# Optimization experiments

Hardware: AMD Instinct MI355X
Metric: run time of the kernel (lower is better)

## Reference

```python
import jax, jax.numpy as jnp
import numpy as np

N_NODES = 50000
N_EDGES = 800000
D_NODE = 128
D_EDGE = 16
HID = 128
BN_EPS = 1e-5


def gcn_conv(h, src, dst, W, b):
    # PyG GCNConv: h' = D^-1/2 (A + I) D^-1/2 (h W) + b, deg includes self-loop
    h = h @ W
    deg = jax.ops.segment_sum(jnp.ones((src.shape[0],), h.dtype), dst,
                              num_segments=N_NODES) + 1.0
    dinv = deg ** -0.5
    norm = dinv[src] * dinv[dst]                      # [E]
    agg = jax.ops.segment_sum(h[src] * norm[:, None], dst,
                              num_segments=N_NODES)   # scatter to dst
    agg = agg + h * (dinv * dinv)[:, None]            # self-loop term
    return agg + b


def setup_inputs() -> dict:
    key = jax.random.key(0)
    ks = jax.random.split(key, 12)
    s = lambda fan_in: 1.0 / np.sqrt(fan_in)
    return {
        "x": jax.random.normal(ks[0], (N_NODES, D_NODE), jnp.float32),
        "edge_index": jax.random.randint(ks[1], (2, N_EDGES), 0, N_NODES, jnp.int32),
        "edge_attr": jax.random.normal(ks[2], (N_EDGES, D_EDGE), jnp.float32),
        "W1": jax.random.normal(ks[3], (D_NODE, HID), jnp.float32) * s(D_NODE),
        "b1": jnp.zeros((HID,), jnp.float32),
        "gamma": jnp.ones((HID,), jnp.float32),
        "beta": jnp.zeros((HID,), jnp.float32),
        "W2": jax.random.normal(ks[4], (HID, HID), jnp.float32) * s(HID),
        "b2": jnp.zeros((HID,), jnp.float32),
        "Wm1": jax.random.normal(ks[5], (2 * HID + D_EDGE, HID), jnp.float32) * s(2 * HID + D_EDGE),
        "bm1": jnp.zeros((HID,), jnp.float32),
        "Wm2": jax.random.normal(ks[6], (HID, 1), jnp.float32) * s(HID),
        "bm2": jnp.zeros((1,), jnp.float32),
    }


def reference(x, edge_index, edge_attr, W1, b1, gamma, beta, W2, b2, Wm1, bm1, Wm2, bm2):
    src, dst = edge_index[0], edge_index[1]
    z = gcn_conv(x, src, dst, W1, b1)
    # BatchNorm1d over nodes (training-mode batch stats, biased var)
    mean = jnp.mean(z, axis=0)
    var = jnp.mean(jnp.square(z - mean), axis=0)
    z = (z - mean) * jax.lax.rsqrt(var + BN_EPS) * gamma + beta
    z = jax.nn.relu(z)
    z = gcn_conv(z, src, dst, W2, b2)
    # edge head: gather endpoints, concat with edge_attr, 2-layer MLP (dropout = eval identity)
    edge_input = jnp.concatenate([z[src], z[dst], edge_attr], axis=1)  # [E, 2H+De]
    h = jax.nn.relu(edge_input @ Wm1 + bm1)
    return (h @ Wm2 + bm2).squeeze(-1)  # [E]
```

## Files before the change

kernel.cpp:

```cpp
#include <hip/hip_runtime.h>
#include <hip/hip_bf16.h>

#define NN 50000
#define NE 800000
#define H 128
#define DE 16
#define BN_EPS 1e-5f
#define NBKT 196
#define NBLK 256
#define EPB 3125
#define EHB 1563

typedef float v2f __attribute__((ext_vector_type(2)));
typedef float v4f __attribute__((ext_vector_type(4)));
typedef short bfrag __attribute__((ext_vector_type(8)));

__device__ __forceinline__ unsigned int packbf2(float a, float b) {
    __hip_bfloat162 h = __float22bfloat162_rn(make_float2(a, b));
    return *(unsigned int*)&h;
}
__device__ __forceinline__ v2f unpackbf2(unsigned int u) {
    v2f r;
    r.x = __uint_as_float(u << 16);
    r.y = __uint_as_float(u & 0xffff0000u);
    return r;
}
__device__ __forceinline__ bfrag cvt8(float4 a0, float4 a1) {
    union { uint4 u; bfrag f; } x;
    x.u.x = packbf2(a0.x, a0.y);
    x.u.y = packbf2(a0.z, a0.w);
    x.u.z = packbf2(a1.x, a1.y);
    x.u.w = packbf2(a1.z, a1.w);
    return x.f;
}
__device__ __forceinline__ bfrag cvt8v(v4f a0, v4f a1) {
    union { uint4 u; bfrag f; } x;
    x.u.x = packbf2(a0.x, a0.y);
    x.u.y = packbf2(a0.z, a0.w);
    x.u.z = packbf2(a1.x, a1.y);
    x.u.w = packbf2(a1.z, a1.w);
    return x.f;
}
#define COMP(u4, j) ((j) == 0 ? (u4).x : (j) == 1 ? (u4).y : (j) == 2 ? (u4).z : (u4).w)

__device__ __forceinline__ float dpp_rowred16(float s) {
    s += __int_as_float(__builtin_amdgcn_update_dpp(0, __float_as_int(s), 0x121, 0xf, 0xf, false));
    s += __int_as_float(__builtin_amdgcn_update_dpp(0, __float_as_int(s), 0x122, 0xf, 0xf, false));
    s += __int_as_float(__builtin_amdgcn_update_dpp(0, __float_as_int(s), 0x124, 0xf, 0xf, false));
    s += __int_as_float(__builtin_amdgcn_update_dpp(0, __float_as_int(s), 0x128, 0xf, 0xf, false));
    return s;
}

__global__ __launch_bounds__(256) void phaseA_k(const int* __restrict__ dst,
                                                int* __restrict__ bhist,
                                                const float* __restrict__ W1,
                                                const float* __restrict__ W2,
                                                const float* __restrict__ Ws,
                                                const float* __restrict__ Wd,
                                                const float* __restrict__ We,
                                                short* __restrict__ d1, short* __restrict__ d2,
                                                short* __restrict__ ds_, short* __restrict__ dd,
                                                unsigned int* __restrict__ WePk) {
    int b = blockIdx.x;
    if (b < NBLK) {
        __shared__ int lh[256];
        lh[threadIdx.x] = 0;
        __syncthreads();
        int base = b * EPB;
        for (int e = threadIdx.x; e < EPB; e += 256)
            atomicAdd(&lh[dst[base + e] >> 8], 1);
        __syncthreads();
        if (threadIdx.x < NBKT)
            bhist[threadIdx.x * NBLK + b] = lh[threadIdx.x];
        return;
    }
    b -= NBLK;
    if (b < 256) {
        int mat = b >> 6;
        const float* s = mat == 0 ? W1 : mat == 1 ? W2 : mat == 2 ? Ws : Wd;
        short* d = mat == 0 ? d1 : mat == 1 ? d2 : mat == 2 ? ds_ : dd;
        int idx = (b & 63) * 256 + threadIdx.x;
        int n = idx & 127, k = idx >> 7;
        float v = s[k * 128 + n];
        d[n * 128 + k] = (short)(packbf2(v, v) & 0xffff);
    } else {
        int idx = (b - 256) * 256 + threadIdx.x;
        int c = idx >> 8;
        int lane = (idx >> 2) & 63;
        int j2 = (idx & 3) * 2;
        int q = lane >> 4, i = lane & 15;
        int k0 = q * 8 + j2, k1 = k0 + 1;
        int feat = i * 8 + c;
        float v0 = (k0 < 16) ? We[k0 * 128 + feat] : 0.f;
        float v1 = (k1 < 16) ? We[k1 * 128 + feat] : 0.f;
        WePk[idx] = packbf2(v0, v1);
    }
}

__global__ void phaseB_k(int* __restrict__ bhist, int* __restrict__ bucketBase,
                         int* __restrict__ bucketTot) {
    __shared__ int sh[256];
    int t = threadIdx.x;
    int tot = 0;
    if (t < NBKT)
        for (int blk = 0; blk < NBLK; blk++) tot += bhist[t * NBLK + blk];
    sh[t] = tot;
    __syncthreads();
    for (int off = 1; off < 256; off <<= 1) {
        int v = (t >= off) ? sh[t - off] : 0;
        __syncthreads();
        sh[t] += v;
        __syncthreads();
    }
    if (t < NBKT) {
        int base = sh[t] - tot;
        bucketBase[t] = base;
        bucketTot[t] = tot;
        int run = base;
        for (int blk = 0; blk < NBLK; blk++) {
            int h = bhist[t * NBLK + blk];
            bhist[t * NBLK + blk] = run;
            run += h;
        }
    }
}

__global__ __launch_bounds__(512) void phaseC_k(const int* __restrict__ src,
                                                const int* __restrict__ dst,
                                                const int* __restrict__ bhist,
                                                unsigned int* __restrict__ tmp) {
    __shared__ int lcur[256];
    int b = blockIdx.x;
    if (threadIdx.x < NBKT)
        lcur[threadIdx.x] = bhist[threadIdx.x * NBLK + b];
    __syncthreads();
    int base = b * EPB;
    for (int e = threadIdx.x; e < EPB; e += 512) {
        int d = dst[base + e];
        int s = src[base + e];
        int pos = atomicAdd(&lcur[d >> 8], 1);
        tmp[pos] = (unsigned int)s | ((unsigned int)(d & 255) << 16);
    }
}

__global__ __launch_bounds__(512) void fillb_k(const int* __restrict__ bucketBase,
                                               const int* __restrict__ bucketTot,
                                               const unsigned int* __restrict__ tmp,
                                               int* __restrict__ counts,
                                               int* __restrict__ offsets,
                                               float* __restrict__ dinv,
                                               int* __restrict__ srcs) {
    __shared__ int hist[256], off[256];
    int t = threadIdx.x;
    int b = blockIdx.x;
    if (t < 256) hist[t] = 0;
    __syncthreads();
    int base = bucketBase[b];
    int tot = bucketTot[b];
    const unsigned int* tp = tmp + base;
    for (int idx = t; idx < tot; idx += 512)
        atomicAdd(&hist[tp[idx] >> 16], 1);
    __syncthreads();
    int h = 0;
    if (t < 256) { h = hist[t]; off[t] = h; }
    __syncthreads();
    for (int o = 1; o < 256; o <<= 1) {
        int v = (t < 256 && t >= o) ? off[t - o] : 0;
        __syncthreads();
        if (t < 256) off[t] += v;
        __syncthreads();
    }
    if (t < 256) {
        int excl = off[t] - h;
        int node = b * 256 + t;
        if (node < NN) {
            counts[node] = h;
            offsets[node] = base + excl;
            dinv[node] = rsqrtf((float)h + 1.0f);
        }
        hist[t] = excl;
    }
    __syncthreads();
    for (int idx = t; idx < tot; idx += 512) {
        unsigned int u = tp[idx];
        int pos = atomicAdd(&hist[u >> 16], 1);
        srcs[base + pos] = (int)(u & 0xffffu);
    }
}

__global__ __launch_bounds__(256) void gemm1_k(const float* __restrict__ A,
                                               const short* __restrict__ Bt,
                                               unsigned int* __restrict__ Cb,
                                               const float* __restrict__ rowScale) {
    int lane = threadIdx.x & 63;
    int w = threadIdx.x >> 6;
    int i = lane & 15;
    int q = lane >> 4;
    int r0 = blockIdx.x * 64 + w * 16;
    int arow = min(r0 + i, NN - 1);
    const float* Arow = A + (size_t)arow * 128;

    v4f acc[8];
#pragma unroll
    for (int c = 0; c < 8; c++) acc[c] = (v4f)0.f;

#pragma unroll
    for (int kc = 0; kc < 128; kc += 32) {
        int kb = kc + q * 8;
        float4 a0 = *(const float4*)&Arow[kb];
        float4 a1 = *(const float4*)&Arow[kb + 4];
        bfrag af = cvt8(a0, a1);
#pragma unroll
        for (int c = 0; c < 8; c++) {
            bfrag bf = *(const bfrag*)&Bt[(size_t)(c * 16 + i) * 128 + kb];
            acc[c] = __builtin_amdgcn_mfma_f32_16x16x32_bf16(af, bf, acc[c], 0, 0, 0);
        }
    }

    int orow0 = r0 + q * 4;
    v4f ds = *(const v4f*)&rowScale[min(orow0, NN - 4)];
#pragma unroll
    for (int c = 0; c < 8; c++) {
        int col = c * 16 + i;
#pragma unroll
        for (int r = 0; r < 4; r++) {
            float v = acc[c][r] * ds[r];
            float vp = __shfl_xor(v, 1, 64);
            if (!(i & 1) && orow0 + r < NN)
                Cb[(size_t)(orow0 + r) * 64 + (col >> 1)] = packbf2(v, vp);
        }
    }
}

__global__ __launch_bounds__(256) void gemm_bn_k(const unsigned int* __restrict__ Ab,
                                                 const short* __restrict__ Bt,
                                                 unsigned int* __restrict__ Cb,
                                                 const float* __restrict__ rowScale,
                                                 const float* __restrict__ sums,
                                                 const float* __restrict__ sumsq,
                                                 const float* __restrict__ gamma,
                                                 const float* __restrict__ beta) {
    __shared__ __align__(16) float tAs[128], tCs[128];
    if (threadIdx.x < 128) {
        int f = threadIdx.x;
        float mean = sums[f] * (1.0f / NN);
        float var = sumsq[f] * (1.0f / NN) - mean * mean;
        float a = gamma[f] * rsqrtf(var + BN_EPS);
        tAs[f] = a;
        tCs[f] = beta[f] - mean * a;
    }
    __syncthreads();

    int lane = threadIdx.x & 63;
    int w = threadIdx.x >> 6;
    int i = lane & 15;
    int q = lane >> 4;
    int r0 = blockIdx.x * 64 + w * 16;
    int arow = min(r0 + i, NN - 1);

    v4f acc[8];
#pragma unroll
    for (int c = 0; c < 8; c++) acc[c] = (v4f)0.f;

#pragma unroll
    for (int kc = 0; kc < 128; kc += 32) {
        int kb = kc + q * 8;
        uint4 u = *(const uint4*)&Ab[(size_t)arow * 64 + (kb >> 1)];
        v2f z0 = unpackbf2(u.x), z1 = unpackbf2(u.y);
        v2f z2 = unpackbf2(u.z), z3 = unpackbf2(u.w);
        v2f t0 = *(const v2f*)&tAs[kb],     c0 = *(const v2f*)&tCs[kb];
        v2f t1 = *(const v2f*)&tAs[kb + 2], c1 = *(const v2f*)&tCs[kb + 2];
        v2f t2 = *(const v2f*)&tAs[kb + 4], c2 = *(const v2f*)&tCs[kb + 4];
        v2f t3 = *(const v2f*)&tAs[kb + 6], c3 = *(const v2f*)&tCs[kb + 6];
        z0 = z0 * t0 + c0; z1 = z1 * t1 + c1;
        z2 = z2 * t2 + c2; z3 = z3 * t3 + c3;
        union { uint4 u; bfrag f; } x;
        x.u.x = packbf2(fmaxf(z0.x, 0.f), fmaxf(z0.y, 0.f));
        x.u.y = packbf2(fmaxf(z1.x, 0.f), fmaxf(z1.y, 0.f));
        x.u.z = packbf2(fmaxf(z2.x, 0.f), fmaxf(z2.y, 0.f));
        x.u.w = packbf2(fmaxf(z3.x, 0.f), fmaxf(z3.y, 0.f));
        bfrag af = x.f;
#pragma unroll
        for (int c = 0; c < 8; c++) {
            bfrag bf = *(const bfrag*)&Bt[(size_t)(c * 16 + i) * 128 + kb];
            acc[c] = __builtin_amdgcn_mfma_f32_16x16x32_bf16(af, bf, acc[c], 0, 0, 0);
        }
    }

    int orow0 = r0 + q * 4;
    v4f ds = *(const v4f*)&rowScale[min(orow0, NN - 4)];
#pragma unroll
    for (int c = 0; c < 8; c++) {
        int col = c * 16 + i;
#pragma unroll
        for (int r = 0; r < 4; r++) {
            float v = acc[c][r] * ds[r];
            float vp = __shfl_xor(v, 1, 64);
            if (!(i & 1) && orow0 + r < NN)
                Cb[(size_t)(orow0 + r) * 64 + (col >> 1)] = packbf2(v, vp);
        }
    }
}

__global__ __launch_bounds__(256) void gemm_pq(const unsigned int* __restrict__ zbA,
                                               const short* __restrict__ Bs_,
                                               const short* __restrict__ Bd_,
                                               const float* __restrict__ bm1,
                                               unsigned int* __restrict__ Pb,
                                               unsigned int* __restrict__ Qb,
                                               int M) {
    int lane = threadIdx.x & 63;
    int w = threadIdx.x >> 6;
    int i = lane & 15;
    int q = lane >> 4;
    int r0 = blockIdx.x * 64 + w * 16;
    int arow = min(r0 + i, M - 1);

    v4f accP[8], accQ[8];
#pragma unroll
    for (int c = 0; c < 8; c++) { accP[c] = (v4f)0.f; accQ[c] = (v4f)0.f; }

#pragma unroll
    for (int kc = 0; kc < 128; kc += 32) {
        int kb = kc + q * 8;
        bfrag af = *(const bfrag*)&zbA[(size_t)arow * 64 + (kb >> 1)];
#pragma unroll
        for (int c = 0; c < 8; c++) {
            bfrag bs = *(const bfrag*)&Bs_[(size_t)(c * 16 + i) * 128 + kb];
            bfrag bd = *(const bfrag*)&Bd_[(size_t)(c * 16 + i) * 128 + kb];
            accP[c] = __builtin_amdgcn_mfma_f32_16x16x32_bf16(af, bs, accP[c], 0, 0, 0);
            accQ[c] = __builtin_amdgcn_mfma_f32_16x16x32_bf16(af, bd, accQ[c], 0, 0, 0);
        }
    }

    int orow0 = r0 + q * 4;
    float bm1c[8];
#pragma unroll
    for (int c = 0; c < 8; c++) bm1c[c] = bm1[c * 16 + i];
#pragma unroll
    for (int c = 0; c < 8; c++) {
        int col = c * 16 + i;
#pragma unroll
        for (int r = 0; r < 4; r++) {
            float vP = accP[c][r];
            float vPp = __shfl_xor(vP, 1, 64);
            float vQ = accQ[c][r] + bm1c[c];
            float vQp = __shfl_xor(vQ, 1, 64);
            if (!(i & 1) && orow0 + r < M) {
                Pb[(size_t)(orow0 + r) * 64 + (col >> 1)] = packbf2(vP, vPp);
                Qb[(size_t)(orow0 + r) * 64 + (col >> 1)] = packbf2(vQ, vQp);
            }
        }
    }
}

__global__ __launch_bounds__(256) void aggregate_k(const unsigned int* __restrict__ hsb,
                                                   const int* __restrict__ offsets,
                                                   const int* __restrict__ counts,
                                                   const int* __restrict__ srcs,
                                                   const float* __restrict__ dinv,
                                                   const float* __restrict__ bias,
                                                   unsigned int* __restrict__ zbout) {
    int lane = threadIdx.x & 63;
    int i = lane & 15;
    int q = lane >> 4;
    int n = __builtin_amdgcn_readfirstlane(blockIdx.x * 4 + (threadIdx.x >> 6));
    if (n >= NN) return;
    int beg = offsets[n];
    int cnt = counts[n];
    v2f A0 = {0.f, 0.f}, A1 = {0.f, 0.f}, A2 = {0.f, 0.f}, A3 = {0.f, 0.f};
    v2f B0 = {0.f, 0.f}, B1 = {0.f, 0.f}, B2 = {0.f, 0.f}, B3 = {0.f, 0.f};
    for (int c = 0; c < cnt; c += 64) {
        int vsrc = srcs[beg + c + lane];
        int m = min(64, cnt - c);
        int ngrp = m >> 2;
        int g = 0;
        for (; g + 4 <= ngrp; g += 4) {
            int s0 = __shfl(vsrc, g * 4 + q, 64);
            int s1 = __shfl(vsrc, g * 4 + 4 + q, 64);
            int s2 = __shfl(vsrc, g * 4 + 8 + q, 64);
            int s3 = __shfl(vsrc, g * 4 + 12 + q, 64);
            uint4 u0 = *(const uint4*)&hsb[(size_t)s0 * 64 + i * 4];
            uint4 u1 = *(const uint4*)&hsb[(size_t)s1 * 64 + i * 4];
            uint4 u2 = *(const uint4*)&hsb[(size_t)s2 * 64 + i * 4];
            uint4 u3 = *(const uint4*)&hsb[(size_t)s3 * 64 + i * 4];
            A0 += unpackbf2(u0.x); A1 += unpackbf2(u0.y); A2 += unpackbf2(u0.z); A3 += unpackbf2(u0.w);
            B0 += unpackbf2(u1.x); B1 += unpackbf2(u1.y); B2 += unpackbf2(u1.z); B3 += unpackbf2(u1.w);
            A0 += unpackbf2(u2.x); A1 += unpackbf2(u2.y); A2 += unpackbf2(u2.z); A3 += unpackbf2(u2.w);
            B0 += unpackbf2(u3.x); B1 += unpackbf2(u3.y); B2 += unpackbf2(u3.z); B3 += unpackbf2(u3.w);
        }
        for (; g < ngrp; g++) {
            int s0 = __shfl(vsrc, g * 4 + q, 64);
            uint4 u0 = *(const uint4*)&hsb[(size_t)s0 * 64 + i * 4];
            A0 += unpackbf2(u0.x); A1 += unpackbf2(u0.y); A2 += unpackbf2(u0.z); A3 += unpackbf2(u0.w);
        }
        int rem = m & 3;
        if (rem) {
            int s0 = __shfl(vsrc, (m & ~3) + q, 64);
            if (q < rem) {
                uint4 u0 = *(const uint4*)&hsb[(size_t)s0 * 64 + i * 4];
                B0 += unpackbf2(u0.x); B1 += unpackbf2(u0.y); B2 += unpackbf2(u0.z); B3 += unpackbf2(u0.w);
            }
        }
    }
    A0 += B0; A1 += B1; A2 += B2; A3 += B3;
    A0.x += __shfl_xor(A0.x, 32, 64); A0.y += __shfl_xor(A0.y, 32, 64);
    A1.x += __shfl_xor(A1.x, 32, 64); A1.y += __shfl_xor(A1.y, 32, 64);
    A2.x += __shfl_xor(A2.x, 32, 64); A2.y += __shfl_xor(A2.y, 32, 64);
    A3.x += __shfl_xor(A3.x, 32, 64); A3.y += __shfl_xor(A3.y, 32, 64);
    bool hi = (lane & 32) != 0;
    v2f U0, U1;
    U0.x = hi ? A2.x : A0.x; U0.y = hi ? A2.y : A0.y;
    U1.x = hi ? A3.x : A1.x; U1.y = hi ? A3.y : A1.y;
    U0.x += __shfl_xor(U0.x, 16, 64); U0.y += __shfl_xor(U0.y, 16, 64);
    U1.x += __shfl_xor(U1.x, 16, 64); U1.y += __shfl_xor(U1.y, 16, 64);
    bool lo = (lane & 16) != 0;
    v2f res;
    res.x = lo ? U1.x : U0.x;
    res.y = lo ? U1.y : U0.y;
    int ui = i * 4 + q;
    v2f self = unpackbf2(hsb[(size_t)n * 64 + ui]);
    float di = dinv[n];
    float2 b = *(const float2*)&bias[ui * 2];
    float rx = (res.x + self.x) * di + b.x;
    float ry = (res.y + self.y) * di + b.y;
    zbout[(size_t)n * 64 + ui] = packbf2(rx, ry);
}

__global__ __launch_bounds__(256) void bnstats_b_k(const unsigned int* __restrict__ zb,
                                                   float* __restrict__ sums,
                                                   float* __restrict__ sumsq) {
    __shared__ v2f ls[4][64], lq[4][64];
    int lane = threadIdx.x & 63;
    int sub = threadIdx.x >> 6;
    v2f s = {0.f, 0.f}, q = {0.f, 0.f};
    for (int r = blockIdx.x * 4 + sub; r < NN; r += gridDim.x * 4) {
        v2f v = unpackbf2(zb[(size_t)r * 64 + lane]);
        s += v;
        q += v * v;
    }
    if (sub) { ls[sub][lane] = s; lq[sub][lane] = q; }
    __syncthreads();
    if (!sub) {
        s += ls[1][lane] + ls[2][lane] + ls[3][lane];
        q += lq[1][lane] + lq[2][lane] + lq[3][lane];
        atomicAdd(&sums[lane * 2], s.x);
        atomicAdd(&sums[lane * 2 + 1], s.y);
        atomicAdd(&sumsq[lane * 2], q.x);
        atomicAdd(&sumsq[lane * 2 + 1], q.y);
    }
}

__global__ __launch_bounds__(256) void edgehead_k(const unsigned int* __restrict__ Pb,
                                                  const unsigned int* __restrict__ Qb,
                                                  const float* __restrict__ ea,
                                                  const int* __restrict__ srcI,
                                                  const int* __restrict__ dstI,
                                                  const unsigned int* __restrict__ WePk,
                                                  const float* __restrict__ Wm2,
                                                  const float* __restrict__ bm2,
                                                  float* __restrict__ out) {
    int lane = threadIdx.x & 63;
    int wid = threadIdx.x >> 6;
    int i = lane & 15;
    int q = lane >> 4;

    bfrag wef[8];
#pragma unroll
    for (int c = 0; c < 8; c++)
        wef[c] = *(const bfrag*)&WePk[(c * 64 + lane) * 4];
    float4 wv0 = *(const float4*)&Wm2[i * 8];
    float4 wv1 = *(const float4*)&Wm2[i * 8 + 4];
    v2f wv2[4];
    wv2[0].x = wv0.x; wv2[0].y = wv0.y;
    wv2[1].x = wv0.z; wv2[1].y = wv0.w;
    wv2[2].x = wv1.x; wv2[2].y = wv1.y;
    wv2[3].x = wv1.z; wv2[3].y = wv1.w;
    float bm2v = bm2[0];

#pragma unroll
    for (int g = 0; g < 2; g++) {
        int base = blockIdx.x * 512 + wid * 128 + g * 64;
        if (base >= NE) break;
        int sv = srcI[base + lane];
        int dv = dstI[base + lane];

#pragma unroll
        for (int t = 0; t < 4; t++) {
            int tb = t * 16;
            bfrag af;
#pragma unroll
            for (int z = 0; z < 8; z++) af[z] = 0;
            if (q < 2) {
                const float* erow = &ea[(size_t)(base + tb + i) * 16 + q * 8];
                v4f e0 = __builtin_nontemporal_load((const v4f*)erow);
                v4f e1 = __builtin_nontemporal_load((const v4f*)(erow + 4));
                af = cvt8v(e0, e1);
            }
            uint4 Pu[4], Qu[4];
#pragma unroll
            for (int r = 0; r < 4; r++) {
                int sr = __shfl(sv, tb + q * 4 + r, 64);
                int dr = __shfl(dv, tb + q * 4 + r, 64);
                Pu[r] = *(const uint4*)&Pb[(size_t)sr * 64 + i * 4];
                Qu[r] = *(const uint4*)&Qb[(size_t)dr * 64 + i * 4];
            }
            v4f acc[8];
#pragma unroll
            for (int c = 0; c < 8; c++) acc[c] = (v4f)0.f;
#pragma unroll
            for (int c = 0; c < 8; c++)
                acc[c] = __builtin_amdgcn_mfma_f32_16x16x32_bf16(af, wef[c], acc[c], 0, 0, 0);
#pragma unroll
            for (int r = 0; r < 4; r++) {
                v2f sa = {0.f, 0.f};
#pragma unroll
                for (int j = 0; j < 4; j++) {
                    v2f pq = unpackbf2(COMP(Pu[r], j)) + unpackbf2(COMP(Qu[r], j));
                    v2f tt;
                    tt.x = acc[2 * j][r] + pq.x;
                    tt.y = acc[2 * j + 1][r] + pq.y;
                    tt.x = fmaxf(tt.x, 0.f);
                    tt.y = fmaxf(tt.y, 0.f);
                    sa += tt * wv2[j];
                }
                float s = dpp_rowred16(sa.x + sa.y);
                if (i == 0) out[base + tb + q * 4 + r] = s + bm2v;
            }
        }
    }
}

extern "C" void kernel_launch(void* const* d_in, const int* in_sizes, int n_in,
                              void* d_out, int out_size, void* d_ws, size_t ws_size,
                              hipStream_t stream) {
    const float* x     = (const float*)d_in[0];
    const int*   ei    = (const int*)d_in[1];
    const float* ea    = (const float*)d_in[2];
    const float* W1    = (const float*)d_in[3];
    const float* b1    = (const float*)d_in[4];
    const float* gamma = (const float*)d_in[5];
    const float* beta  = (const float*)d_in[6];
    const float* W2    = (const float*)d_in[7];
    const float* b2    = (const float*)d_in[8];
    const float* Wm1   = (const float*)d_in[9];
    const float* bm1   = (const float*)d_in[10];
    const float* Wm2   = (const float*)d_in[11];
    const float* bm2   = (const float*)d_in[12];
    float* out = (float*)d_out;

    const int* srcI = ei;
    const int* dstI = ei + NE;

    char* w = (char*)d_ws;
    auto alloc = [&](size_t bytes) {
        char* p = w;
        w += (bytes + 255) & ~(size_t)255;
        return p;
    };
    float* sums    = (float*)alloc(256 * 4);
    float* sumsq   = sums + 128;
    int*   bhist   = (int*)alloc(NBKT * NBLK * 4);
    int*   bucketBase = (int*)alloc(NBKT * 4);
    int*   bucketTot  = (int*)alloc(NBKT * 4);
    unsigned int* tmp = (unsigned int*)alloc((size_t)NE * 4);
    int*   counts  = (int*)alloc(NN * 4);
    int*   offsets = (int*)alloc(NN * 4);
    float* dinv    = (float*)alloc(NN * 4);
    int*   srcs    = (int*)alloc((size_t)(NE + 64) * 4);
    short* bt1     = (short*)alloc(128 * 128 * 2);
    short* bt2     = (short*)alloc(128 * 128 * 2);
    short* bts     = (short*)alloc(128 * 128 * 2);
    short* btd     = (short*)alloc(128 * 128 * 2);
    unsigned int* WePk = (unsigned int*)alloc(2048 * 4);
    unsigned int* hsb  = (unsigned int*)alloc((size_t)NN * 64 * 4);
    unsigned int* zb1  = (unsigned int*)alloc((size_t)NN * 64 * 4);
    unsigned int* Qb   = (unsigned int*)alloc((size_t)NN * 64 * 4);
    unsigned int* zb2  = zb1;

    hipMemsetAsync(sums, 0, 256 * 4, stream);

    phaseA_k<<<NBLK + 264, 256, 0, stream>>>(dstI, bhist, W1, W2, Wm1,
                                             Wm1 + 128 * 128, Wm1 + 256 * 128,
                                             bt1, bt2, bts, btd, WePk);
    phaseB_k<<<1, 256, 0, stream>>>(bhist, bucketBase, bucketTot);
    phaseC_k<<<NBLK, 512, 0, stream>>>(srcI, dstI, bhist, tmp);
    fillb_k<<<NBKT, 512, 0, stream>>>(bucketBase, bucketTot, tmp,
                                      counts, offsets, dinv, srcs);

    const int GB = (NN + 63) / 64;
    const int AGG = (NN + 3) / 4;

    gemm1_k<<<GB, 256, 0, stream>>>(x, bt1, hsb, dinv);
    aggregate_k<<<AGG, 256, 0, stream>>>(hsb, offsets, counts, srcs, dinv, b1, zb1);
    bnstats_b_k<<<256, 256, 0, stream>>>(zb1, sums, sumsq);
    gemm_bn_k<<<GB, 256, 0, stream>>>(zb1, bt2, hsb, dinv, sums, sumsq, gamma, beta);
    aggregate_k<<<AGG, 256, 0, stream>>>(hsb, offsets, counts, srcs, dinv, b2, zb2);
    gemm_pq<<<GB, 256, 0, stream>>>(zb2, bts, btd, bm1, hsb, Qb, NN);
    edgehead_k<<<EHB, 256, 0, stream>>>(hsb, Qb, ea, srcI, dstI, WePk,
                                        Wm2, bm2, out);
}
```

Before: 405.1 us.

## Split GCN aggregation into four feature-slice passes and flatten edge-head grid

The neighbor aggregation now runs as four launches, each gathering only a 64-byte column slice of every source row, with 16 edges in flight per wave and a shuffle reduction over rows. The aim is to shrink the per-pass gather working set so it stays resident in cache, at the cost of re-reading the CSR indices four times and doing four times as many launches. Separately, the edge-head kernel drops its two-iteration per-wave loop so each wave handles one 64-edge tile, which doubles the grid, and its output writes use nontemporal stores.

```diff
diff --git a/kernel.cpp b/kernel.cpp
--- a/kernel.cpp
+++ b/kernel.cpp
@@ -6,10 +6,10 @@
 #define H 128
 #define DE 16
 #define BN_EPS 1e-5f
+#define NB_E 3125
 #define NBKT 196
 #define NBLK 256
 #define EPB 3125
-#define EHB 1563
 
 typedef float v2f __attribute__((ext_vector_type(2)));
 typedef float v4f __attribute__((ext_vector_type(4)));
@@ -354,77 +354,65 @@
     }
 }
 
-__global__ __launch_bounds__(256) void aggregate_k(const unsigned int* __restrict__ hsb,
-                                                   const int* __restrict__ offsets,
-                                                   const int* __restrict__ counts,
-                                                   const int* __restrict__ srcs,
-                                                   const float* __restrict__ dinv,
-                                                   const float* __restrict__ bias,
-                                                   unsigned int* __restrict__ zbout) {
+__global__ __launch_bounds__(256) void aggslice_k(const unsigned int* __restrict__ hsb,
+                                                  const int* __restrict__ offsets,
+                                                  const int* __restrict__ counts,
+                                                  const int* __restrict__ srcs,
+                                                  const float* __restrict__ dinv,
+                                                  const float* __restrict__ bias,
+                                                  unsigned int* __restrict__ zbout,
+                                                  int sl) {
     int lane = threadIdx.x & 63;
-    int i = lane & 15;
-    int q = lane >> 4;
+    int row = lane >> 2;
+    int c = lane & 3;
     int n = __builtin_amdgcn_readfirstlane(blockIdx.x * 4 + (threadIdx.x >> 6));
     if (n >= NN) return;
     int beg = offsets[n];
     int cnt = counts[n];
-    v2f A0 = {0.f, 0.f}, A1 = {0.f, 0.f}, A2 = {0.f, 0.f}, A3 = {0.f, 0.f};
-    v2f B0 = {0.f, 0.f}, B1 = {0.f, 0.f}, B2 = {0.f, 0.f}, B3 = {0.f, 0.f};
-    for (int c = 0; c < cnt; c += 64) {
-        int vsrc = srcs[beg + c + lane];
-        int m = min(64, cnt - c);
-        int ngrp = m >> 2;
-        int g = 0;
-        for (; g + 4 <= ngrp; g += 4) {
-            int s0 = __shfl(vsrc, g * 4 + q, 64);
-            int s1 = __shfl(vsrc, g * 4 + 4 + q, 64);
-            int s2 = __shfl(vsrc, g * 4 + 8 + q, 64);
-            int s3 = __shfl(vsrc, g * 4 + 12 + q, 64);
-            uint4 u0 = *(const uint4*)&hsb[(size_t)s0 * 64 + i * 4];
-            uint4 u1 = *(const uint4*)&hsb[(size_t)s1 * 64 + i * 4];
-            uint4 u2 = *(const uint4*)&hsb[(size_t)s2 * 64 + i * 4];
-            uint4 u3 = *(const uint4*)&hsb[(size_t)s3 * 64 + i * 4];
-            A0 += unpackbf2(u0.x); A1 += unpackbf2(u0.y); A2 += unpackbf2(u0.z); A3 += unpackbf2(u0.w);
-            B0 += unpackbf2(u1.x); B1 += unpackbf2(u1.y); B2 += unpackbf2(u1.z); B3 += unpackbf2(u1.w);
-            A0 += unpackbf2(u2.x); A1 += unpackbf2(u2.y); A2 += unpackbf2(u2.z); A3 += unpackbf2(u2.w);
-            B0 += unpackbf2(u3.x); B1 += unpackbf2(u3.y); B2 += unpackbf2(u3.z); B3 += unpackbf2(u3.w);
-        }
-        for (; g < ngrp; g++) {
-            int s0 = __shfl(vsrc, g * 4 + q, 64);
-            uint4 u0 = *(const uint4*)&hsb[(size_t)s0 * 64 + i * 4];
-            A0 += unpackbf2(u0.x); A1 += unpackbf2(u0.y); A2 += unpackbf2(u0.z); A3 += unpackbf2(u0.w);
-        }
-        int rem = m & 3;
+    const unsigned int* hcol = hsb + sl * 16 + c * 4;
+    v2f a0 = {0.f, 0.f}, a1 = {0.f, 0.f}, a2 = {0.f, 0.f}, a3 = {0.f, 0.f};
+    for (int cc = 0; cc < cnt; cc += 64) {
+        int vsrc = srcs[beg + cc + lane];
+        int m = min(64, cnt - cc);
+        int ng = m >> 4;
+        for (int g = 0; g < ng; g++) {
+            int sr = __shfl(vsrc, g * 16 + row, 64);
+            uint4 u = *(const uint4*)&hcol[(size_t)sr * 64];
+            a0 += unpackbf2(u.x); a1 += unpackbf2(u.y);
+            a2 += unpackbf2(u.z); a3 += unpackbf2(u.w);
+        }
+        int rem = m & 15;
         if (rem) {
-            int s0 = __shfl(vsrc, (m & ~3) + q, 64);
-            if (q < rem) {
-                uint4 u0 = *(const uint4*)&hsb[(size_t)s0 * 64 + i * 4];
-                B0 += unpackbf2(u0.x); B1 += unpackbf2(u0.y); B2 += unpackbf2(u0.z); B3 += unpackbf2(u0.w);
+            int sr = __shfl(vsrc, (m & ~15) + row, 64);
+            if (row < rem) {
+                uint4 u = *(const uint4*)&hcol[(size_t)sr * 64];
+                a0 += unpackbf2(u.x); a1 += unpackbf2(u.y);
+                a2 += unpackbf2(u.z); a3 += unpackbf2(u.w);
             }
         }
     }
-    A0 += B0; A1 += B1; A2 += B2; A3 += B3;
-    A0.x += __shfl_xor(A0.x, 32, 64); A0.y += __shfl_xor(A0.y, 32, 64);
-    A1.x += __shfl_xor(A1.x, 32, 64); A1.y += __shfl_xor(A1.y, 32, 64);
-    A2.x += __shfl_xor(A2.x, 32, 64); A2.y += __shfl_xor(A2.y, 32, 64);
-    A3.x += __shfl_xor(A3.x, 32, 64); A3.y += __shfl_xor(A3.y, 32, 64);
-    bool hi = (lane & 32) != 0;
-    v2f U0, U1;
-    U0.x = hi ? A2.x : A0.x; U0.y = hi ? A2.y : A0.y;
-    U1.x = hi ? A3.x : A1.x; U1.y = hi ? A3.y : A1.y;
-    U0.x += __shfl_xor(U0.x, 16, 64); U0.y += __shfl_xor(U0.y, 16, 64);
-    U1.x += __shfl_xor(U1.x, 16, 64); U1.y += __shfl_xor(U1.y, 16, 64);
-    bool lo = (lane & 16) != 0;
-    v2f res;
-    res.x = lo ? U1.x : U0.x;
-    res.y = lo ? U1.y : U0.y;
-    int ui = i * 4 + q;
-    v2f self = unpackbf2(hsb[(size_t)n * 64 + ui]);
-    float di = dinv[n];
-    float2 b = *(const float2*)&bias[ui * 2];
-    float rx = (res.x + self.x) * di + b.x;
-    float ry = (res.y + self.y) * di + b.y;
-    zbout[(size_t)n * 64 + ui] = packbf2(rx, ry);
+#pragma unroll
+    for (int off = 4; off <= 32; off <<= 1) {
+        a0.x += __shfl_xor(a0.x, off, 64); a0.y += __shfl_xor(a0.y, off, 64);
+        a1.x += __shfl_xor(a1.x, off, 64); a1.y += __shfl_xor(a1.y, off, 64);
+        a2.x += __shfl_xor(a2.x, off, 64); a2.y += __shfl_xor(a2.y, off, 64);
+        a3.x += __shfl_xor(a3.x, off, 64); a3.y += __shfl_xor(a3.y, off, 64);
+    }
+    if (row == 0) {
+        uint4 su = *(const uint4*)&hcol[(size_t)n * 64];
+        v2f s0 = unpackbf2(su.x), s1 = unpackbf2(su.y);
+        v2f s2 = unpackbf2(su.z), s3 = unpackbf2(su.w);
+        float di = dinv[n];
+        int fb = sl * 32 + c * 8;
+        float4 b0 = *(const float4*)&bias[fb];
+        float4 b1 = *(const float4*)&bias[fb + 4];
+        uint4 o;
+        o.x = packbf2((a0.x + s0.x) * di + b0.x, (a0.y + s0.y) * di + b0.y);
+        o.y = packbf2((a1.x + s1.x) * di + b0.z, (a1.y + s1.y) * di + b0.w);
+        o.z = packbf2((a2.x + s2.x) * di + b1.x, (a2.y + s2.y) * di + b1.y);
+        o.w = packbf2((a3.x + s3.x) * di + b1.z, (a3.y + s3.y) * di + b1.w);
+        *(uint4*)&zbout[(size_t)n * 64 + sl * 16 + c * 4] = o;
+    }
 }
 
 __global__ __launch_bounds__(256) void bnstats_b_k(const unsigned int* __restrict__ zb,
@@ -462,6 +450,7 @@
                                                   float* __restrict__ out) {
     int lane = threadIdx.x & 63;
     int wid = threadIdx.x >> 6;
+    int base = (blockIdx.x * 4 + wid) * 64;
     int i = lane & 15;
     int q = lane >> 4;
 
@@ -478,55 +467,50 @@
     wv2[3].x = wv1.z; wv2[3].y = wv1.w;
     float bm2v = bm2[0];
 
-#pragma unroll
-    for (int g = 0; g < 2; g++) {
-        int base = blockIdx.x * 512 + wid * 128 + g * 64;
-        if (base >= NE) break;
-        int sv = srcI[base + lane];
-        int dv = dstI[base + lane];
-
-#pragma unroll
-        for (int t = 0; t < 4; t++) {
-            int tb = t * 16;
-            bfrag af;
-#pragma unroll
-            for (int z = 0; z < 8; z++) af[z] = 0;
-            if (q < 2) {
-                const float* erow = &ea[(size_t)(base + tb + i) * 16 + q * 8];
-                v4f e0 = __builtin_nontemporal_load((const v4f*)erow);
-                v4f e1 = __builtin_nontemporal_load((const v4f*)(erow + 4));
-                af = cvt8v(e0, e1);
+    int sv = srcI[base + lane];
+    int dv = dstI[base + lane];
+
+#pragma unroll
+    for (int t = 0; t < 4; t++) {
+        int tb = t * 16;
+        bfrag af;
+#pragma unroll
+        for (int z = 0; z < 8; z++) af[z] = 0;
+        if (q < 2) {
+            const float* erow = &ea[(size_t)(base + tb + i) * 16 + q * 8];
+            v4f e0 = __builtin_nontemporal_load((const v4f*)erow);
+            v4f e1 = __builtin_nontemporal_load((const v4f*)(erow + 4));
+            af = cvt8v(e0, e1);
+        }
+        uint4 Pu[4], Qu[4];
+#pragma unroll
+        for (int r = 0; r < 4; r++) {
+            int sr = __shfl(sv, tb + q * 4 + r, 64);
+            int dr = __shfl(dv, tb + q * 4 + r, 64);
+            Pu[r] = *(const uint4*)&Pb[(size_t)sr * 64 + i * 4];
+            Qu[r] = *(const uint4*)&Qb[(size_t)dr * 64 + i * 4];
+        }
+        v4f acc[8];
+#pragma unroll
+        for (int c = 0; c < 8; c++) acc[c] = (v4f)0.f;
+#pragma unroll
+        for (int c = 0; c < 8; c++)
+            acc[c] = __builtin_amdgcn_mfma_f32_16x16x32_bf16(af, wef[c], acc[c], 0, 0, 0);
+#pragma unroll
+        for (int r = 0; r < 4; r++) {
+            v2f sa = {0.f, 0.f};
+#pragma unroll
+            for (int j = 0; j < 4; j++) {
+                v2f pq = unpackbf2(COMP(Pu[r], j)) + unpackbf2(COMP(Qu[r], j));
+                v2f tt;
+                tt.x = acc[2 * j][r] + pq.x;
+                tt.y = acc[2 * j + 1][r] + pq.y;
+                tt.x = fmaxf(tt.x, 0.f);
+                tt.y = fmaxf(tt.y, 0.f);
+                sa += tt * wv2[j];
             }
-            uint4 Pu[4], Qu[4];
-#pragma unroll
-            for (int r = 0; r < 4; r++) {
-                int sr = __shfl(sv, tb + q * 4 + r, 64);
-                int dr = __shfl(dv, tb + q * 4 + r, 64);
-                Pu[r] = *(const uint4*)&Pb[(size_t)sr * 64 + i * 4];
-                Qu[r] = *(const uint4*)&Qb[(size_t)dr * 64 + i * 4];
-            }
-            v4f acc[8];
-#pragma unroll
-            for (int c = 0; c < 8; c++) acc[c] = (v4f)0.f;
-#pragma unroll
-            for (int c = 0; c < 8; c++)
-                acc[c] = __builtin_amdgcn_mfma_f32_16x16x32_bf16(af, wef[c], acc[c], 0, 0, 0);
-#pragma unroll
-            for (int r = 0; r < 4; r++) {
-                v2f sa = {0.f, 0.f};
-#pragma unroll
-                for (int j = 0; j < 4; j++) {
-                    v2f pq = unpackbf2(COMP(Pu[r], j)) + unpackbf2(COMP(Qu[r], j));
-                    v2f tt;
-                    tt.x = acc[2 * j][r] + pq.x;
-                    tt.y = acc[2 * j + 1][r] + pq.y;
-                    tt.x = fmaxf(tt.x, 0.f);
-                    tt.y = fmaxf(tt.y, 0.f);
-                    sa += tt * wv2[j];
-                }
-                float s = dpp_rowred16(sa.x + sa.y);
-                if (i == 0) out[base + tb + q * 4 + r] = s + bm2v;
-            }
+            float s = dpp_rowred16(sa.x + sa.y);
+            if (i == 0) __builtin_nontemporal_store(s + bm2v, &out[base + tb + q * 4 + r]);
         }
     }
 }
@@ -592,11 +576,15 @@
     const int AGG = (NN + 3) / 4;
 
     gemm1_k<<<GB, 256, 0, stream>>>(x, bt1, hsb, dinv);
-    aggregate_k<<<AGG, 256, 0, stream>>>(hsb, offsets, counts, srcs, dinv, b1, zb1);
+    for (int sl = 0; sl < 4; sl++)
+        aggslice_k<<<AGG, 256, 0, stream>>>(hsb, offsets, counts, srcs, dinv, b1,
+                                            zb1, sl);
     bnstats_b_k<<<256, 256, 0, stream>>>(zb1, sums, sumsq);
     gemm_bn_k<<<GB, 256, 0, stream>>>(zb1, bt2, hsb, dinv, sums, sumsq, gamma, beta);
-    aggregate_k<<<AGG, 256, 0, stream>>>(hsb, offsets, counts, srcs, dinv, b2, zb2);
+    for (int sl = 0; sl < 4; sl++)
+        aggslice_k<<<AGG, 256, 0, stream>>>(hsb, offsets, counts, srcs, dinv, b2,
+                                            zb2, sl);
     gemm_pq<<<GB, 256, 0, stream>>>(zb2, bts, btd, bm1, hsb, Qb, NN);
-    edgehead_k<<<EHB, 256, 0, stream>>>(hsb, Qb, ea, srcI, dstI, WePk,
-                                        Wm2, bm2, out);
-}
+    edgehead_k<<<NB_E, 256, 0, stream>>>(hsb, Qb, ea, srcI, dstI, WePk,
+                                         Wm2, bm2, out);
+}
```

Measured after the change: 518.9 us. 28.1% more time.
